# Kernel tuning notes

Measured on AMD Instinct MI355X. Metric: run time of the kernel, lower is better.

The kernel has to match this reference:

```python
import jax, jax.numpy as jnp
import numpy as np

B, S, H, DH = 8, 2048, 4, 32
D = H * DH  # all_head_size = true_hidden_size = 128


def setup_inputs() -> dict:
    key = jax.random.key(0)
    ks = jax.random.split(key, 9)
    inp = {
        "query_tensor": jax.random.normal(ks[0], (B, S, D), dtype=jnp.float32),
        "key_tensor": jax.random.normal(ks[1], (B, S, D), dtype=jnp.float32),
        "value_tensor": jax.random.normal(ks[2], (B, S, D), dtype=jnp.float32),
        "attention_mask": jnp.zeros((B, 1, 1, S), dtype=jnp.float32),
        "head_mask": jnp.ones((1, H, 1, 1), dtype=jnp.float32),
        "Wq": jax.random.normal(ks[3], (D, D), dtype=jnp.float32) * 0.02,
        "bq": jnp.zeros((D,), dtype=jnp.float32),
        "Wk": jax.random.normal(ks[4], (D, D), dtype=jnp.float32) * 0.02,
        "bk": jnp.zeros((D,), dtype=jnp.float32),
        "Wv": jax.random.normal(ks[5], (D, D), dtype=jnp.float32) * 0.02,
        "bv": jnp.zeros((D,), dtype=jnp.float32),
    }
    return inp


def _split_heads(x):
    # (B, S, D) -> (B, H, S, DH)
    return x.reshape(B, S, H, DH).transpose(0, 2, 1, 3)


def reference(query_tensor, key_tensor, value_tensor, attention_mask, head_mask,
              Wq, bq, Wk, bk, Wv, bv):
    q = _split_heads(query_tensor @ Wq + bq)   # (B,H,S,DH)
    k = _split_heads(key_tensor @ Wk + bk)
    v = _split_heads(value_tensor @ Wv + bv)

    scale = 1.0 / jnp.sqrt(jnp.float32(DH))
    scores = jnp.einsum("bhqd,bhkd->bhqk", q, k) * scale + attention_mask
    probs = jax.nn.softmax(scores, axis=-1)
    # dropout is identity at inference (training=False)
    probs = probs * head_mask
    ctx = jnp.einsum("bhqk,bhkd->bhqd", probs, v)  # (B,H,S,DH)
    ctx = ctx.transpose(0, 2, 1, 3).reshape(B, S, D)
    return ctx
```

## Files before the change

kernel.cpp:

```cpp
#include <hip/hip_runtime.h>
#include <hip/hip_bf16.h>
#include <math.h>

#define B_ 8
#define S_ 2048
#define H_ 4
#define DH_ 32
#define D_ 128
#define BS_ (B_ * S_)
#define NT_ 32
#define LOG2E 1.4426950408889634f
#define QSCALE (0.17677669529663687f * LOG2E)

typedef float f32x4 __attribute__((ext_vector_type(4)));
typedef short s16x8 __attribute__((ext_vector_type(8)));

__device__ __forceinline__ unsigned short bf(float x) {
    return __builtin_bit_cast(unsigned short, __float2bfloat16(x));
}
__device__ __forceinline__ float bf2f(unsigned short u) {
    return __builtin_bit_cast(float, (unsigned int)u << 16);
}
__device__ __forceinline__ unsigned int pk2(float a, float b) {
    return (unsigned int)bf(a) | ((unsigned int)bf(b) << 16);
}
__device__ __forceinline__ void gll16(const void* g, void* l) {
    __builtin_amdgcn_global_load_lds(
        (const __attribute__((address_space(1))) unsigned int*)(g),
        (__attribute__((address_space(3))) unsigned int*)(l), 16, 0, 0);
}

__global__ __launch_bounds__(256) void wprep(
    const float* __restrict__ Wq, const float* __restrict__ Wk, const float* __restrict__ Wv,
    const float* __restrict__ maskg,
    unsigned short* __restrict__ Wt, unsigned short* __restrict__ Em)
{
    if (blockIdx.z == 3) {
        const int id16 = blockIdx.y * 4 + blockIdx.x;
        const int base = id16 * 1024 + threadIdx.x * 4;
        float4 m4 = *(const float4*)&maskg[base];
        ushort4 o;
        o.x = bf(__builtin_amdgcn_exp2f(m4.x * LOG2E));
        o.y = bf(__builtin_amdgcn_exp2f(m4.y * LOG2E));
        o.z = bf(__builtin_amdgcn_exp2f(m4.z * LOG2E));
        o.w = bf(__builtin_amdgcn_exp2f(m4.w * LOG2E));
        *(ushort4*)&Em[base] = o;
        return;
    }
    const float* W = (blockIdx.z == 0) ? Wq : (blockIdx.z == 1) ? Wk : Wv;
    unsigned short* Oh = Wt + (size_t)blockIdx.z * D_ * D_;
    unsigned short* Ol = Oh + 3 * D_ * D_;
    __shared__ float tf[32][36];
    const int t = threadIdx.x;
    const int kt = blockIdx.x * 32, ct = blockIdx.y * 32;
    {
        int kl = t >> 3, cl = (t & 7) * 4;
        float4 w4 = *(const float4*)&W[(size_t)(kt + kl) * D_ + ct + cl];
        tf[kl][cl + 0] = w4.x; tf[kl][cl + 1] = w4.y;
        tf[kl][cl + 2] = w4.z; tf[kl][cl + 3] = w4.w;
    }
    __syncthreads();
    {
        int cl = t >> 3, kl = (t & 7) * 4;
        ushort4 oh, ol;
        float v;
        v = tf[kl + 0][cl]; oh.x = bf(v); ol.x = bf(v - bf2f(oh.x));
        v = tf[kl + 1][cl]; oh.y = bf(v); ol.y = bf(v - bf2f(oh.y));
        v = tf[kl + 2][cl]; oh.z = bf(v); ol.z = bf(v - bf2f(oh.z));
        v = tf[kl + 3][cl]; oh.w = bf(v); ol.w = bf(v - bf2f(oh.w));
        *(ushort4*)&Oh[(size_t)(ct + cl) * D_ + kt + kl] = oh;
        *(ushort4*)&Ol[(size_t)(ct + cl) * D_ + kt + kl] = ol;
    }
}

__global__ __launch_bounds__(256) void qkv_mfma(
    const float* __restrict__ Xq, const float* __restrict__ Xk, const float* __restrict__ Xv,
    const unsigned short* __restrict__ Wt, const float* __restrict__ maskg,
    const float* __restrict__ bq, const float* __restrict__ bk, const float* __restrict__ bv,
    unsigned short* __restrict__ Qo, unsigned short* __restrict__ Ko,
    unsigned short* __restrict__ Vt)
{
    const int mode = blockIdx.z, chalf = blockIdx.y;
    const float* X; const float* bias; unsigned short* O; float scl;
    if (mode == 0)      { X = Xq; bias = bq; O = Qo; scl = QSCALE; }
    else if (mode == 1) { X = Xk; bias = bk; O = Ko; scl = 1.f; }
    else                { X = Xv; bias = bv; O = Vt; scl = 1.f; }
    const unsigned short* WmH = Wt + (size_t)mode * D_ * D_;
    const unsigned short* WmL = WmH + 3 * D_ * D_;

    __shared__ __align__(16) unsigned short xa[2 * 32 * 136];
    __shared__ __align__(16) unsigned short wt[2 * 64 * 136];

    const int t = threadIdx.x;
    const long row0 = (long)blockIdx.x * 32;

    #pragma unroll
    for (int j = 0; j < 8; j++) {
        int idx = t + 256 * j;
        int part = idx >> 10, i2 = idx & 1023;
        int r = i2 >> 4, c16 = i2 & 15;
        const unsigned short* src = part ? WmL : WmH;
        uint4 v = *(const uint4*)&src[(size_t)(chalf * 64 + r) * D_ + c16 * 8];
        *(uint4*)&wt[part * 8704 + r * 136 + c16 * 8] = v;
    }
    #pragma unroll
    for (int j = 0; j < 4; j++) {
        int idx = t + 256 * j;
        int r = idx >> 5, c4 = idx & 31;
        float4 v = *(const float4*)(X + (row0 + r) * D_ + c4 * 4);
        ushort4 ph, pl;
        ph.x = bf(v.x); pl.x = bf(v.x - bf2f(ph.x));
        ph.y = bf(v.y); pl.y = bf(v.y - bf2f(ph.y));
        ph.z = bf(v.z); pl.z = bf(v.z - bf2f(ph.z));
        ph.w = bf(v.w); pl.w = bf(v.w - bf2f(ph.w));
        *(ushort4*)&xa[r * 136 + c4 * 4] = ph;
        *(ushort4*)&xa[4352 + r * 136 + c4 * 4] = pl;
    }
    __syncthreads();

    const int w = t >> 6, lane = t & 63, lo = lane & 15, hi = lane >> 4;
    const int mf = w >> 1, nb = (w & 1) * 2;
    f32x4 acc[2] = {};
    #pragma unroll
    for (int kk = 0; kk < 4; kk++) {
        const int ko = kk * 32 + hi * 8;
        s16x8 ah = *(const s16x8*)&xa[(mf * 16 + lo) * 136 + ko];
        s16x8 al = *(const s16x8*)&xa[4352 + (mf * 16 + lo) * 136 + ko];
        #pragma unroll
        for (int n2 = 0; n2 < 2; n2++) {
            const int nf = nb + n2;
            s16x8 bh2 = *(const s16x8*)&wt[(nf * 16 + lo) * 136 + ko];
            s16x8 bl2 = *(const s16x8*)&wt[8704 + (nf * 16 + lo) * 136 + ko];
            acc[n2] = __builtin_amdgcn_mfma_f32_16x16x32_bf16(ah, bh2, acc[n2], 0, 0, 0);
            acc[n2] = __builtin_amdgcn_mfma_f32_16x16x32_bf16(al, bh2, acc[n2], 0, 0, 0);
            acc[n2] = __builtin_amdgcn_mfma_f32_16x16x32_bf16(ah, bl2, acc[n2], 0, 0, 0);
        }
    }
    __syncthreads();

    if (mode < 2) {
        #pragma unroll
        for (int n2 = 0; n2 < 2; n2++) {
            int c_l = (nb + n2) * 16 + lo;
            float bb = bias[chalf * 64 + c_l];
            #pragma unroll
            for (int r = 0; r < 4; r++) {
                int s = mf * 16 + hi * 4 + r;
                xa[s * 72 + c_l] = bf((acc[n2][r] + bb) * scl);
            }
        }
        __syncthreads();
        int s = t >> 3, part = t & 7;
        int c_g = chalf * 64 + part * 8;
        int h = c_g >> 5, d = c_g & 31;
        long b_i = (row0 + s) >> 11, s_i = (row0 + s) & 2047;
        unsigned short* orow = O + ((b_i * H_ + h) * (long)S_ + s_i) * DH_ + d;
        *(uint4*)orow = *(const uint4*)&xa[s * 72 + part * 8];
    } else {
        const long b_i = row0 >> 11;
        const long s0g = row0 & 2047;
        float emr[4];
        #pragma unroll
        for (int r = 0; r < 4; r++) {
            const int s_l = mf * 16 + hi * 4 + r;
            emr[r] = __builtin_amdgcn_exp2f(maskg[b_i * S_ + s0g + s_l] * LOG2E);
        }
        #pragma unroll
        for (int n2 = 0; n2 < 2; n2++) {
            int c_l = (nb + n2) * 16 + lo;
            float bb = bias[chalf * 64 + c_l];
            #pragma unroll
            for (int r = 0; r < 4; r++) {
                int s = mf * 16 + hi * 4 + r;
                xa[c_l * 68 + s] = bf((acc[n2][r] + bb) * emr[r]);
            }
        }
        __syncthreads();
        if (t < 128) {
            int c_l = t >> 1, sh2 = (t & 1) * 16;
            int c_g = chalf * 64 + c_l;
            int h = c_g >> 5, d = c_g & 31;
            long s_i = s0g + sh2;
            unsigned short* orow = O + ((b_i * H_ + h) * (long)DH_ + d) * S_ + s_i;
            uint2 p0 = *(const uint2*)&xa[c_l * 68 + sh2 + 0];
            uint2 p1 = *(const uint2*)&xa[c_l * 68 + sh2 + 4];
            uint2 p2 = *(const uint2*)&xa[c_l * 68 + sh2 + 8];
            uint2 p3 = *(const uint2*)&xa[c_l * 68 + sh2 + 12];
            *(uint4*)&orow[0] = make_uint4(p0.x, p0.y, p1.x, p1.y);
            *(uint4*)&orow[8] = make_uint4(p2.x, p2.y, p3.x, p3.y);
        }
    }
}

__global__ __launch_bounds__(256) void flash_mfma(
    const unsigned short* __restrict__ Qg, const unsigned short* __restrict__ Kg,
    const unsigned short* __restrict__ Vtg, const unsigned short* __restrict__ Emg,
    const float* __restrict__ head_mask, float* __restrict__ Out)
{
    __shared__ __align__(16) unsigned short ks[2][64][32];
    __shared__ __align__(16) unsigned short vs[2][32][72];
    __shared__ __align__(16) unsigned short ps[4][16][72];

    const int t = threadIdx.x, w = t >> 6, lane = t & 63;
    const int lo = lane & 15, hi = lane >> 4;

    const int lid = blockIdx.x;
    const int xcd = lid & 7, ser = lid >> 3;
    const int bh = xcd + 8 * (ser >> 5);
    const int qi = ser & 31;
    const int b = bh >> 2, h = bh & 3;

    const size_t kvbase = (size_t)bh * S_ * DH_;
    const size_t vtbase = (size_t)bh * DH_ * S_;
    const unsigned short* emb = Emg + (size_t)b * S_;
    const int q0 = qi * 64 + w * 16;

    s16x8 qf = *(const s16x8*)(Qg + kvbase + (size_t)(q0 + lo) * DH_ + hi * 8);

    const float hm = head_mask[h];
    const int vd = t >> 3, vk = (t & 7) * 8;
    const int krow = lane >> 2, kchunk = (lane & 3) ^ (krow & 3);
    const size_t koff = (size_t)(w * 16 + krow) * DH_ + kchunk * 8;

    gll16(Kg + kvbase + koff, &ks[0][w * 16][0]);
    *(uint4*)&vs[0][vd][vk] = *(const uint4*)(Vtg + vtbase + (size_t)vd * S_ + vk);
    __syncthreads();

    f32x4 ctx[2] = {};
    f32x4 lacc = {};
    const f32x4 z4 = {0.f, 0.f, 0.f, 0.f};
    uint4 vreg;

    const int kread = (hi ^ (lo & 3)) * 8;

    for (int tile = 0; tile < NT_; tile++) {
        const int cur = tile & 1, nxt = cur ^ 1;

        if (tile < NT_ - 1) {
            gll16(Kg + kvbase + (size_t)(tile + 1) * 64 * DH_ + koff, &ks[nxt][w * 16][0]);
            vreg = *(const uint4*)(Vtg + vtbase + (size_t)vd * S_ + (tile + 1) * 64 + vk);
        }
        s16x8 ef0 = *(const s16x8*)(emb + tile * 64 + hi * 8);
        s16x8 ef1 = *(const s16x8*)(emb + tile * 64 + 32 + hi * 8);

        __builtin_amdgcn_s_setprio(1);
        #pragma unroll
        for (int mt = 0; mt < 4; mt++) {
            s16x8 kf = *(const s16x8*)&ks[cur][mt * 16 + lo][kread];
            f32x4 d = __builtin_amdgcn_mfma_f32_16x16x32_bf16(kf, qf, z4, 0, 0, 0);
            float p0 = __builtin_amdgcn_exp2f(d[0]);
            float p1 = __builtin_amdgcn_exp2f(d[1]);
            float p2 = __builtin_amdgcn_exp2f(d[2]);
            float p3 = __builtin_amdgcn_exp2f(d[3]);
            uint2 u = make_uint2(pk2(p0, p1), pk2(p2, p3));
            *(uint2*)&ps[w][lo][mt * 16 + hi * 4] = u;
        }
        __builtin_amdgcn_s_setprio(0);

        __builtin_amdgcn_s_setprio(1);
        #pragma unroll
        for (int k2 = 0; k2 < 2; k2++) {
            s16x8 pa = *(const s16x8*)&ps[w][lo][k2 * 32 + hi * 8];
            lacc = __builtin_amdgcn_mfma_f32_16x16x32_bf16(pa, k2 ? ef1 : ef0, lacc, 0, 0, 0);
            #pragma unroll
            for (int nd = 0; nd < 2; nd++) {
                s16x8 vb = *(const s16x8*)&vs[cur][nd * 16 + lo][k2 * 32 + hi * 8];
                ctx[nd] = __builtin_amdgcn_mfma_f32_16x16x32_bf16(pa, vb, ctx[nd], 0, 0, 0);
            }
        }
        __builtin_amdgcn_s_setprio(0);

        if (tile < NT_ - 1) {
            *(uint4*)&vs[nxt][vd][vk] = vreg;
            __syncthreads();
        }
    }

    f32x4 inv;
    #pragma unroll
    for (int r = 0; r < 4; r++) inv[r] = hm / lacc[r];
    #pragma unroll
    for (int nd = 0; nd < 2; nd++) {
        #pragma unroll
        for (int r = 0; r < 4; r++) {
            size_t sq = (size_t)q0 + hi * 4 + r;
            Out[((size_t)b * S_ + sq) * D_ + h * DH_ + nd * 16 + lo] = ctx[nd][r] * inv[r];
        }
    }
}

extern "C" void kernel_launch(void* const* d_in, const int* in_sizes, int n_in,
                              void* d_out, int out_size, void* d_ws, size_t ws_size,
                              hipStream_t stream) {
    const float* Xq   = (const float*)d_in[0];
    const float* Xk   = (const float*)d_in[1];
    const float* Xv   = (const float*)d_in[2];
    const float* mask = (const float*)d_in[3];
    const float* hm   = (const float*)d_in[4];
    const float* Wq   = (const float*)d_in[5];
    const float* bq   = (const float*)d_in[6];
    const float* Wk   = (const float*)d_in[7];
    const float* bk   = (const float*)d_in[8];
    const float* Wv   = (const float*)d_in[9];
    const float* bv   = (const float*)d_in[10];
    float* out = (float*)d_out;

    unsigned short* Qo = (unsigned short*)d_ws;
    unsigned short* Ko = Qo + (size_t)2097152;
    unsigned short* Vt = Ko + (size_t)2097152;
    unsigned short* Wt = Vt + (size_t)2097152;
    unsigned short* Em = Wt + (size_t)98304;

    wprep<<<dim3(4, 4, 4), 256, 0, stream>>>(Wq, Wk, Wv, mask, Wt, Em);
    qkv_mfma<<<dim3(BS_ / 32, 2, 3), 256, 0, stream>>>(Xq, Xk, Xv, Wt, mask, bq, bk, bv, Qo, Ko, Vt);
    flash_mfma<<<dim3(1024), 256, 0, stream>>>(Qo, Ko, Vt, Em, hm, out);
}
```

Baseline: 62.84 us.

## Rewrite flash attention with 32x32 MFMA, register K, permlane P reuse, additive mask

Switches the attention kernel from 16x16x32 to 32x32x16 bf16 MFMA tiles, with each wave handling 32 query rows and each block 128 queries, which halves the grid. K fragments are now loaded straight into registers instead of through LDS, and probabilities are reshuffled in registers with v_permlane32_swap rather than staged through an LDS buffer. The mask becomes an additive log2 term inside exp2 instead of a multiplicative factor applied to V and the row sum, and the row sum is computed by an MFMA against a ones vector. This removes LDS round-trips and barriers for P and K, at the cost of higher register pressure, a grid of 512 blocks, and duplicated MFMA work for the denominator.

```diff
diff --git a/kernel.cpp b/kernel.cpp
--- a/kernel.cpp
+++ b/kernel.cpp
@@ -12,8 +12,9 @@
 #define LOG2E 1.4426950408889634f
 #define QSCALE (0.17677669529663687f * LOG2E)
 
-typedef float f32x4 __attribute__((ext_vector_type(4)));
-typedef short s16x8 __attribute__((ext_vector_type(8)));
+typedef float f32x4  __attribute__((ext_vector_type(4)));
+typedef float f32x16 __attribute__((ext_vector_type(16)));
+typedef short s16x8  __attribute__((ext_vector_type(8)));
 
 __device__ __forceinline__ unsigned short bf(float x) {
     return __builtin_bit_cast(unsigned short, __float2bfloat16(x));
@@ -24,27 +25,21 @@
 __device__ __forceinline__ unsigned int pk2(float a, float b) {
     return (unsigned int)bf(a) | ((unsigned int)bf(b) << 16);
 }
-__device__ __forceinline__ void gll16(const void* g, void* l) {
-    __builtin_amdgcn_global_load_lds(
-        (const __attribute__((address_space(1))) unsigned int*)(g),
-        (__attribute__((address_space(3))) unsigned int*)(l), 16, 0, 0);
+__device__ __forceinline__ void pswap(unsigned int& a, unsigned int& b) {
+    asm volatile("v_permlane32_swap_b32 %0, %1" : "+v"(a), "+v"(b));
 }
 
 __global__ __launch_bounds__(256) void wprep(
     const float* __restrict__ Wq, const float* __restrict__ Wk, const float* __restrict__ Wv,
     const float* __restrict__ maskg,
-    unsigned short* __restrict__ Wt, unsigned short* __restrict__ Em)
+    unsigned short* __restrict__ Wt, float* __restrict__ Eml)
 {
     if (blockIdx.z == 3) {
         const int id16 = blockIdx.y * 4 + blockIdx.x;
         const int base = id16 * 1024 + threadIdx.x * 4;
         float4 m4 = *(const float4*)&maskg[base];
-        ushort4 o;
-        o.x = bf(__builtin_amdgcn_exp2f(m4.x * LOG2E));
-        o.y = bf(__builtin_amdgcn_exp2f(m4.y * LOG2E));
-        o.z = bf(__builtin_amdgcn_exp2f(m4.z * LOG2E));
-        o.w = bf(__builtin_amdgcn_exp2f(m4.w * LOG2E));
-        *(ushort4*)&Em[base] = o;
+        float4 o = make_float4(m4.x * LOG2E, m4.y * LOG2E, m4.z * LOG2E, m4.w * LOG2E);
+        *(float4*)&Eml[base] = o;
         return;
     }
     const float* W = (blockIdx.z == 0) ? Wq : (blockIdx.z == 1) ? Wk : Wv;
@@ -75,7 +70,7 @@
 
 __global__ __launch_bounds__(256) void qkv_mfma(
     const float* __restrict__ Xq, const float* __restrict__ Xk, const float* __restrict__ Xv,
-    const unsigned short* __restrict__ Wt, const float* __restrict__ maskg,
+    const unsigned short* __restrict__ Wt,
     const float* __restrict__ bq, const float* __restrict__ bk, const float* __restrict__ bv,
     unsigned short* __restrict__ Qo, unsigned short* __restrict__ Ko,
     unsigned short* __restrict__ Vt)
@@ -159,12 +154,6 @@
     } else {
         const long b_i = row0 >> 11;
         const long s0g = row0 & 2047;
-        float emr[4];
-        #pragma unroll
-        for (int r = 0; r < 4; r++) {
-            const int s_l = mf * 16 + hi * 4 + r;
-            emr[r] = __builtin_amdgcn_exp2f(maskg[b_i * S_ + s0g + s_l] * LOG2E);
-        }
         #pragma unroll
         for (int n2 = 0; n2 < 2; n2++) {
             int c_l = (nb + n2) * 16 + lo;
@@ -172,7 +161,7 @@
             #pragma unroll
             for (int r = 0; r < 4; r++) {
                 int s = mf * 16 + hi * 4 + r;
-                xa[c_l * 68 + s] = bf((acc[n2][r] + bb) * emr[r]);
+                xa[c_l * 68 + s] = bf(acc[n2][r] + bb);
             }
         }
         __syncthreads();
@@ -194,98 +183,112 @@
 
 __global__ __launch_bounds__(256) void flash_mfma(
     const unsigned short* __restrict__ Qg, const unsigned short* __restrict__ Kg,
-    const unsigned short* __restrict__ Vtg, const unsigned short* __restrict__ Emg,
+    const unsigned short* __restrict__ Vtg, const float* __restrict__ Eml,
     const float* __restrict__ head_mask, float* __restrict__ Out)
 {
-    __shared__ __align__(16) unsigned short ks[2][64][32];
     __shared__ __align__(16) unsigned short vs[2][32][72];
-    __shared__ __align__(16) unsigned short ps[4][16][72];
 
     const int t = threadIdx.x, w = t >> 6, lane = t & 63;
-    const int lo = lane & 15, hi = lane >> 4;
+    const int l31 = lane & 31, hw = lane >> 5;
 
     const int lid = blockIdx.x;
     const int xcd = lid & 7, ser = lid >> 3;
-    const int bh = xcd + 8 * (ser >> 5);
-    const int qi = ser & 31;
+    const int bh = xcd + 8 * (ser >> 4);
+    const int qi = ser & 15;
     const int b = bh >> 2, h = bh & 3;
 
     const size_t kvbase = (size_t)bh * S_ * DH_;
     const size_t vtbase = (size_t)bh * DH_ * S_;
-    const unsigned short* emb = Emg + (size_t)b * S_;
-    const int q0 = qi * 64 + w * 16;
-
-    s16x8 qf = *(const s16x8*)(Qg + kvbase + (size_t)(q0 + lo) * DH_ + hi * 8);
-
+    const float* emlb = Eml + (size_t)b * S_;
+    const int q0 = qi * 128 + w * 32;
     const float hm = head_mask[h];
+
+    const unsigned short* qp = Qg + kvbase + (size_t)(q0 + l31) * DH_ + hw * 8;
+    const s16x8 qf0 = *(const s16x8*)qp;
+    const s16x8 qf1 = *(const s16x8*)(qp + 16);
+
+    const unsigned short* kfp = Kg + kvbase + (size_t)l31 * DH_ + hw * 8;
+    s16x8 kf00 = *(const s16x8*)(kfp);
+    s16x8 kf01 = *(const s16x8*)(kfp + 16);
+    s16x8 kf10 = *(const s16x8*)(kfp + 1024);
+    s16x8 kf11 = *(const s16x8*)(kfp + 1040);
+
     const int vd = t >> 3, vk = (t & 7) * 8;
-    const int krow = lane >> 2, kchunk = (lane & 3) ^ (krow & 3);
-    const size_t koff = (size_t)(w * 16 + krow) * DH_ + kchunk * 8;
-
-    gll16(Kg + kvbase + koff, &ks[0][w * 16][0]);
     *(uint4*)&vs[0][vd][vk] = *(const uint4*)(Vtg + vtbase + (size_t)vd * S_ + vk);
     __syncthreads();
 
-    f32x4 ctx[2] = {};
-    f32x4 lacc = {};
-    const f32x4 z4 = {0.f, 0.f, 0.f, 0.f};
-    uint4 vreg;
-
-    const int kread = (hi ^ (lo & 3)) * 8;
+    f32x16 ctx = {};
+    f32x16 lacc = {};
+    const f32x16 z16 = {};
+    const s16x8 ones = {0x3F80, 0x3F80, 0x3F80, 0x3F80, 0x3F80, 0x3F80, 0x3F80, 0x3F80};
 
     for (int tile = 0; tile < NT_; tile++) {
         const int cur = tile & 1, nxt = cur ^ 1;
 
+        s16x8 kn00, kn01, kn10, kn11; uint4 vreg;
         if (tile < NT_ - 1) {
-            gll16(Kg + kvbase + (size_t)(tile + 1) * 64 * DH_ + koff, &ks[nxt][w * 16][0]);
+            const unsigned short* kp2 = kfp + (size_t)(tile + 1) * 2048;
+            kn00 = *(const s16x8*)(kp2);
+            kn01 = *(const s16x8*)(kp2 + 16);
+            kn10 = *(const s16x8*)(kp2 + 1024);
+            kn11 = *(const s16x8*)(kp2 + 1040);
             vreg = *(const uint4*)(Vtg + vtbase + (size_t)vd * S_ + (tile + 1) * 64 + vk);
         }
-        s16x8 ef0 = *(const s16x8*)(emb + tile * 64 + hi * 8);
-        s16x8 ef1 = *(const s16x8*)(emb + tile * 64 + 32 + hi * 8);
-
-        __builtin_amdgcn_s_setprio(1);
-        #pragma unroll
-        for (int mt = 0; mt < 4; mt++) {
-            s16x8 kf = *(const s16x8*)&ks[cur][mt * 16 + lo][kread];
-            f32x4 d = __builtin_amdgcn_mfma_f32_16x16x32_bf16(kf, qf, z4, 0, 0, 0);
-            float p0 = __builtin_amdgcn_exp2f(d[0]);
-            float p1 = __builtin_amdgcn_exp2f(d[1]);
-            float p2 = __builtin_amdgcn_exp2f(d[2]);
-            float p3 = __builtin_amdgcn_exp2f(d[3]);
-            uint2 u = make_uint2(pk2(p0, p1), pk2(p2, p3));
-            *(uint2*)&ps[w][lo][mt * 16 + hi * 4] = u;
-        }
-        __builtin_amdgcn_s_setprio(0);
-
-        __builtin_amdgcn_s_setprio(1);
-        #pragma unroll
-        for (int k2 = 0; k2 < 2; k2++) {
-            s16x8 pa = *(const s16x8*)&ps[w][lo][k2 * 32 + hi * 8];
-            lacc = __builtin_amdgcn_mfma_f32_16x16x32_bf16(pa, k2 ? ef1 : ef0, lacc, 0, 0, 0);
+        const float* emt = emlb + tile * 64 + hw * 4;
+        f32x4 ea[4], eb[4];
+        #pragma unroll
+        for (int g = 0; g < 4; g++) {
+            ea[g] = *(const f32x4*)(emt + g * 8);
+            eb[g] = *(const f32x4*)(emt + 32 + g * 8);
+        }
+
+        #pragma unroll
+        for (int kgrp = 0; kgrp < 2; kgrp++) {
+            const s16x8 ka = kgrp ? kf10 : kf00;
+            const s16x8 kb = kgrp ? kf11 : kf01;
+
+            __builtin_amdgcn_s_setprio(1);
+            f32x16 s = __builtin_amdgcn_mfma_f32_32x32x16_bf16(ka, qf0, z16, 0, 0, 0);
+            s = __builtin_amdgcn_mfma_f32_32x32x16_bf16(kb, qf1, s, 0, 0, 0);
+            __builtin_amdgcn_s_setprio(0);
+
+            unsigned int pd[8];
             #pragma unroll
-            for (int nd = 0; nd < 2; nd++) {
-                s16x8 vb = *(const s16x8*)&vs[cur][nd * 16 + lo][k2 * 32 + hi * 8];
-                ctx[nd] = __builtin_amdgcn_mfma_f32_16x16x32_bf16(pa, vb, ctx[nd], 0, 0, 0);
+            for (int j = 0; j < 8; j++) {
+                const int r0 = 2 * j, r1 = 2 * j + 1;
+                const float e0 = kgrp ? eb[r0 >> 2][r0 & 3] : ea[r0 >> 2][r0 & 3];
+                const float e1 = kgrp ? eb[r1 >> 2][r1 & 3] : ea[r1 >> 2][r1 & 3];
+                const float p0 = __builtin_amdgcn_exp2f(s[r0] + e0);
+                const float p1 = __builtin_amdgcn_exp2f(s[r1] + e1);
+                pd[j] = pk2(p0, p1);
             }
-        }
-        __builtin_amdgcn_s_setprio(0);
+            pswap(pd[0], pd[2]); pswap(pd[1], pd[3]);
+            pswap(pd[4], pd[6]); pswap(pd[5], pd[7]);
+            const s16x8 pa0 = __builtin_bit_cast(s16x8, make_uint4(pd[0], pd[1], pd[2], pd[3]));
+            const s16x8 pa1 = __builtin_bit_cast(s16x8, make_uint4(pd[4], pd[5], pd[6], pd[7]));
+
+            __builtin_amdgcn_s_setprio(1);
+            const s16x8 vb0 = *(const s16x8*)&vs[cur][l31][kgrp * 32 + hw * 8];
+            ctx  = __builtin_amdgcn_mfma_f32_32x32x16_bf16(pa0, vb0, ctx, 0, 0, 0);
+            lacc = __builtin_amdgcn_mfma_f32_32x32x16_bf16(pa0, ones, lacc, 0, 0, 0);
+            const s16x8 vb1 = *(const s16x8*)&vs[cur][l31][kgrp * 32 + 16 + hw * 8];
+            ctx  = __builtin_amdgcn_mfma_f32_32x32x16_bf16(pa1, vb1, ctx, 0, 0, 0);
+            lacc = __builtin_amdgcn_mfma_f32_32x32x16_bf16(pa1, ones, lacc, 0, 0, 0);
+            __builtin_amdgcn_s_setprio(0);
+        }
 
         if (tile < NT_ - 1) {
             *(uint4*)&vs[nxt][vd][vk] = vreg;
             __syncthreads();
-        }
-    }
-
-    f32x4 inv;
+            kf00 = kn00; kf01 = kn01; kf10 = kn10; kf11 = kn11;
+        }
+    }
+
     #pragma unroll
-    for (int r = 0; r < 4; r++) inv[r] = hm / lacc[r];
-    #pragma unroll
-    for (int nd = 0; nd < 2; nd++) {
-        #pragma unroll
-        for (int r = 0; r < 4; r++) {
-            size_t sq = (size_t)q0 + hi * 4 + r;
-            Out[((size_t)b * S_ + sq) * D_ + h * DH_ + nd * 16 + lo] = ctx[nd][r] * inv[r];
-        }
+    for (int r = 0; r < 16; r++) {
+        const int qrow = (r & 3) + 8 * (r >> 2) + 4 * hw;
+        const float inv = hm / lacc[r];
+        Out[((size_t)b * S_ + q0 + qrow) * D_ + h * DH_ + l31] = ctx[r] * inv;
     }
 }
 
@@ -309,9 +312,9 @@
     unsigned short* Ko = Qo + (size_t)2097152;
     unsigned short* Vt = Ko + (size_t)2097152;
     unsigned short* Wt = Vt + (size_t)2097152;
-    unsigned short* Em = Wt + (size_t)98304;
-
-    wprep<<<dim3(4, 4, 4), 256, 0, stream>>>(Wq, Wk, Wv, mask, Wt, Em);
-    qkv_mfma<<<dim3(BS_ / 32, 2, 3), 256, 0, stream>>>(Xq, Xk, Xv, Wt, mask, bq, bk, bv, Qo, Ko, Vt);
-    flash_mfma<<<dim3(1024), 256, 0, stream>>>(Qo, Ko, Vt, Em, hm, out);
-}
+    float*          Eml = (float*)((char*)d_ws + 12779520);
+
+    wprep<<<dim3(4, 4, 4), 256, 0, stream>>>(Wq, Wk, Wv, mask, Wt, Eml);
+    qkv_mfma<<<dim3(BS_ / 32, 2, 3), 256, 0, stream>>>(Xq, Xk, Xv, Wt, bq, bk, bv, Qo, Ko, Vt);
+    flash_mfma<<<dim3(512), 256, 0, stream>>>(Qo, Ko, Vt, Eml, hm, out);
+}
```

New measurement: 73.61 us. +17.1%, slower.

## Rewrite attention with 32x32 MFMA, fragment-ordered K/V layout and split-K waves

Applied to the files above, without the earlier changes.

The QKV projection now writes K and V straight into MFMA fragment order, so the attention kernel loads its operands from global memory into registers with no LDS staging or barriers in the main loop. The attention kernel switches to 32x32x16 MFMA with 32 query rows per block. The four waves split the key range and are combined through an LDS reduction at the end. P is repacked with v_cvt_pk_bf16_f32 and v_permlane32_swap instead of a round trip through LDS. This removes the per-tile LDS traffic and syncs, at the cost of a doubled grid, a final cross-wave reduction, and more register pressure.

```diff
diff --git a/kernel.cpp b/kernel.cpp
--- a/kernel.cpp
+++ b/kernel.cpp
@@ -8,12 +8,12 @@
 #define DH_ 32
 #define D_ 128
 #define BS_ (B_ * S_)
-#define NT_ 32
 #define LOG2E 1.4426950408889634f
 #define QSCALE (0.17677669529663687f * LOG2E)
 
-typedef float f32x4 __attribute__((ext_vector_type(4)));
-typedef short s16x8 __attribute__((ext_vector_type(8)));
+typedef float f32x4  __attribute__((ext_vector_type(4)));
+typedef float f32x16 __attribute__((ext_vector_type(16)));
+typedef short s16x8  __attribute__((ext_vector_type(8)));
 
 __device__ __forceinline__ unsigned short bf(float x) {
     return __builtin_bit_cast(unsigned short, __float2bfloat16(x));
@@ -22,13 +22,19 @@
     return __builtin_bit_cast(float, (unsigned int)u << 16);
 }
 __device__ __forceinline__ unsigned int pk2(float a, float b) {
-    return (unsigned int)bf(a) | ((unsigned int)bf(b) << 16);
-}
-__device__ __forceinline__ void gll16(const void* g, void* l) {
-    __builtin_amdgcn_global_load_lds(
-        (const __attribute__((address_space(1))) unsigned int*)(g),
-        (__attribute__((address_space(3))) unsigned int*)(l), 16, 0, 0);
-}
+    unsigned int r;
+    asm("v_cvt_pk_bf16_f32 %0, %1, %2" : "=v"(r) : "v"(a), "v"(b));
+    return r;
+}
+__device__ __forceinline__ void pswap(unsigned int& a, unsigned int& b) {
+    asm volatile("v_permlane32_swap_b32 %0, %1" : "+v"(a), "+v"(b));
+}
+
+#define OFF_Q  0u
+#define OFF_K  2097152u
+#define OFF_V  4194304u
+#define OFF_W  6291456u
+#define OFF_E  6389760u
 
 __global__ __launch_bounds__(256) void wprep(
     const float* __restrict__ Wq, const float* __restrict__ Wk, const float* __restrict__ Wv,
@@ -77,14 +83,14 @@
     const float* __restrict__ Xq, const float* __restrict__ Xk, const float* __restrict__ Xv,
     const unsigned short* __restrict__ Wt, const float* __restrict__ maskg,
     const float* __restrict__ bq, const float* __restrict__ bk, const float* __restrict__ bv,
-    unsigned short* __restrict__ Qo, unsigned short* __restrict__ Ko,
-    unsigned short* __restrict__ Vt)
+    unsigned short* __restrict__ Qo, unsigned short* __restrict__ Kf,
+    unsigned short* __restrict__ Vf)
 {
     const int mode = blockIdx.z, chalf = blockIdx.y;
-    const float* X; const float* bias; unsigned short* O; float scl;
-    if (mode == 0)      { X = Xq; bias = bq; O = Qo; scl = QSCALE; }
-    else if (mode == 1) { X = Xk; bias = bk; O = Ko; scl = 1.f; }
-    else                { X = Xv; bias = bv; O = Vt; scl = 1.f; }
+    const float* X; const float* bias; float scl;
+    if (mode == 0)      { X = Xq; bias = bq; scl = QSCALE; }
+    else if (mode == 1) { X = Xk; bias = bk; scl = 1.f; }
+    else                { X = Xv; bias = bv; scl = 1.f; }
     const unsigned short* WmH = Wt + (size_t)mode * D_ * D_;
     const unsigned short* WmL = WmH + 3 * D_ * D_;
 
@@ -138,6 +144,9 @@
     }
     __syncthreads();
 
+    const long b_i = row0 >> 11;
+    const long s0g = row0 & 2047;
+
     if (mode < 2) {
         #pragma unroll
         for (int n2 = 0; n2 < 2; n2++) {
@@ -152,13 +161,19 @@
         __syncthreads();
         int s = t >> 3, part = t & 7;
         int c_g = chalf * 64 + part * 8;
-        int h = c_g >> 5, d = c_g & 31;
-        long b_i = (row0 + s) >> 11, s_i = (row0 + s) & 2047;
-        unsigned short* orow = O + ((b_i * H_ + h) * (long)S_ + s_i) * DH_ + d;
-        *(uint4*)orow = *(const uint4*)&xa[s * 72 + part * 8];
+        int h = c_g >> 5, dd = c_g & 31;
+        long s_i = s0g + s;
+        int bh = (int)(b_i * H_ + h);
+        uint4 val = *(const uint4*)&xa[s * 72 + part * 8];
+        if (mode == 0) {
+            *(uint4*)(Qo + ((size_t)bh * S_ + s_i) * DH_ + dd) = val;
+        } else {
+            int fr = dd >> 4, hwd = (dd >> 3) & 1;
+            size_t off = ((((size_t)bh * 64 + (s_i >> 5)) * 2 + fr) * 64
+                          + (s_i & 31) + hwd * 32) * 8;
+            *(uint4*)(Kf + off) = val;
+        }
     } else {
-        const long b_i = row0 >> 11;
-        const long s0g = row0 & 2047;
         float emr[4];
         #pragma unroll
         for (int r = 0; r < 4; r++) {
@@ -179,112 +194,116 @@
         if (t < 128) {
             int c_l = t >> 1, sh2 = (t & 1) * 16;
             int c_g = chalf * 64 + c_l;
-            int h = c_g >> 5, d = c_g & 31;
-            long s_i = s0g + sh2;
-            unsigned short* orow = O + ((b_i * H_ + h) * (long)DH_ + d) * S_ + s_i;
+            int h = c_g >> 5, dd = c_g & 31;
+            long key0 = s0g + sh2;
+            int bh = (int)(b_i * H_ + h);
+            size_t base = (((size_t)bh * 128 + (key0 >> 4)) * 64 + dd) * 8;
             uint2 p0 = *(const uint2*)&xa[c_l * 68 + sh2 + 0];
             uint2 p1 = *(const uint2*)&xa[c_l * 68 + sh2 + 4];
             uint2 p2 = *(const uint2*)&xa[c_l * 68 + sh2 + 8];
             uint2 p3 = *(const uint2*)&xa[c_l * 68 + sh2 + 12];
-            *(uint4*)&orow[0] = make_uint4(p0.x, p0.y, p1.x, p1.y);
-            *(uint4*)&orow[8] = make_uint4(p2.x, p2.y, p3.x, p3.y);
-        }
-    }
-}
-
-__global__ __launch_bounds__(256) void flash_mfma(
-    const unsigned short* __restrict__ Qg, const unsigned short* __restrict__ Kg,
-    const unsigned short* __restrict__ Vtg, const unsigned short* __restrict__ Emg,
+            *(uint4*)(Vf + base)       = make_uint4(p0.x, p0.y, p1.x, p1.y);
+            *(uint4*)(Vf + base + 256) = make_uint4(p2.x, p2.y, p3.x, p3.y);
+        }
+    }
+}
+
+__global__ __launch_bounds__(256, 4) void flash_mfma(
+    const unsigned short* __restrict__ Qg, const unsigned short* __restrict__ Kfg,
+    const unsigned short* __restrict__ Vfg, const unsigned short* __restrict__ Emg,
     const float* __restrict__ head_mask, float* __restrict__ Out)
 {
-    __shared__ __align__(16) unsigned short ks[2][64][32];
-    __shared__ __align__(16) unsigned short vs[2][32][72];
-    __shared__ __align__(16) unsigned short ps[4][16][72];
+    __shared__ float ms[2][64][33];
 
     const int t = threadIdx.x, w = t >> 6, lane = t & 63;
-    const int lo = lane & 15, hi = lane >> 4;
+    const int l31 = lane & 31, hw = lane >> 5;
 
     const int lid = blockIdx.x;
     const int xcd = lid & 7, ser = lid >> 3;
-    const int bh = xcd + 8 * (ser >> 5);
-    const int qi = ser & 31;
+    const int bh = xcd * 4 + (ser >> 6);
+    const int qi = ser & 63;
     const int b = bh >> 2, h = bh & 3;
-
-    const size_t kvbase = (size_t)bh * S_ * DH_;
-    const size_t vtbase = (size_t)bh * DH_ * S_;
-    const unsigned short* emb = Emg + (size_t)b * S_;
-    const int q0 = qi * 64 + w * 16;
-
-    s16x8 qf = *(const s16x8*)(Qg + kvbase + (size_t)(q0 + lo) * DH_ + hi * 8);
-
-    const float hm = head_mask[h];
-    const int vd = t >> 3, vk = (t & 7) * 8;
-    const int krow = lane >> 2, kchunk = (lane & 3) ^ (krow & 3);
-    const size_t koff = (size_t)(w * 16 + krow) * DH_ + kchunk * 8;
-
-    gll16(Kg + kvbase + koff, &ks[0][w * 16][0]);
-    *(uint4*)&vs[0][vd][vk] = *(const uint4*)(Vtg + vtbase + (size_t)vd * S_ + vk);
-    __syncthreads();
-
-    f32x4 ctx[2] = {};
-    f32x4 lacc = {};
-    const f32x4 z4 = {0.f, 0.f, 0.f, 0.f};
-    uint4 vreg;
-
-    const int kread = (hi ^ (lo & 3)) * 8;
-
-    for (int tile = 0; tile < NT_; tile++) {
-        const int cur = tile & 1, nxt = cur ^ 1;
-
-        if (tile < NT_ - 1) {
-            gll16(Kg + kvbase + (size_t)(tile + 1) * 64 * DH_ + koff, &ks[nxt][w * 16][0]);
-            vreg = *(const uint4*)(Vtg + vtbase + (size_t)vd * S_ + (tile + 1) * 64 + vk);
-        }
-        s16x8 ef0 = *(const s16x8*)(emb + tile * 64 + hi * 8);
-        s16x8 ef1 = *(const s16x8*)(emb + tile * 64 + 32 + hi * 8);
-
-        __builtin_amdgcn_s_setprio(1);
-        #pragma unroll
-        for (int mt = 0; mt < 4; mt++) {
-            s16x8 kf = *(const s16x8*)&ks[cur][mt * 16 + lo][kread];
-            f32x4 d = __builtin_amdgcn_mfma_f32_16x16x32_bf16(kf, qf, z4, 0, 0, 0);
-            float p0 = __builtin_amdgcn_exp2f(d[0]);
-            float p1 = __builtin_amdgcn_exp2f(d[1]);
-            float p2 = __builtin_amdgcn_exp2f(d[2]);
-            float p3 = __builtin_amdgcn_exp2f(d[3]);
-            uint2 u = make_uint2(pk2(p0, p1), pk2(p2, p3));
-            *(uint2*)&ps[w][lo][mt * 16 + hi * 4] = u;
-        }
-        __builtin_amdgcn_s_setprio(0);
-
-        __builtin_amdgcn_s_setprio(1);
-        #pragma unroll
-        for (int k2 = 0; k2 < 2; k2++) {
-            s16x8 pa = *(const s16x8*)&ps[w][lo][k2 * 32 + hi * 8];
-            lacc = __builtin_amdgcn_mfma_f32_16x16x32_bf16(pa, k2 ? ef1 : ef0, lacc, 0, 0, 0);
-            #pragma unroll
-            for (int nd = 0; nd < 2; nd++) {
-                s16x8 vb = *(const s16x8*)&vs[cur][nd * 16 + lo][k2 * 32 + hi * 8];
-                ctx[nd] = __builtin_amdgcn_mfma_f32_16x16x32_bf16(pa, vb, ctx[nd], 0, 0, 0);
-            }
-        }
-        __builtin_amdgcn_s_setprio(0);
-
-        if (tile < NT_ - 1) {
-            *(uint4*)&vs[nxt][vd][vk] = vreg;
-            __syncthreads();
-        }
-    }
-
-    f32x4 inv;
-    #pragma unroll
-    for (int r = 0; r < 4; r++) inv[r] = hm / lacc[r];
-    #pragma unroll
-    for (int nd = 0; nd < 2; nd++) {
-        #pragma unroll
-        for (int r = 0; r < 4; r++) {
-            size_t sq = (size_t)q0 + hi * 4 + r;
-            Out[((size_t)b * S_ + sq) * D_ + h * DH_ + nd * 16 + lo] = ctx[nd][r] * inv[r];
+    const int q0 = qi * 32;
+
+    const unsigned short* qp = Qg + ((size_t)bh * S_ + q0 + l31) * DH_ + hw * 8;
+    const s16x8 qf0 = *(const s16x8*)qp;
+    const s16x8 qf1 = *(const s16x8*)(qp + 16);
+
+    const unsigned short* kp = Kfg + (size_t)bh * 65536 + (size_t)w * 1024 + (size_t)lane * 8;
+    const unsigned short* vp = Vfg + (size_t)bh * 65536 + (size_t)w * 1024 + (size_t)lane * 8;
+    const unsigned short* ep = Emg + (size_t)b * S_ + w * 32 + hw * 8;
+
+    s16x8 kf0 = *(const s16x8*)kp;
+    s16x8 kf1 = *(const s16x8*)(kp + 512);
+    s16x8 vf0 = *(const s16x8*)vp;
+    s16x8 vf1 = *(const s16x8*)(vp + 512);
+
+    f32x16 ctx = {}, lacc = {};
+    const f32x16 z16 = {};
+
+    for (int tile = 0; tile < 16; tile++) {
+        s16x8 kn0, kn1, vn0, vn1;
+        if (tile < 15) {
+            const unsigned short* kp2 = kp + (size_t)(tile + 1) * 4096;
+            const unsigned short* vp2 = vp + (size_t)(tile + 1) * 4096;
+            kn0 = *(const s16x8*)kp2;
+            kn1 = *(const s16x8*)(kp2 + 512);
+            vn0 = *(const s16x8*)vp2;
+            vn1 = *(const s16x8*)(vp2 + 512);
+        }
+        const s16x8 ef0 = *(const s16x8*)(ep + tile * 128);
+        const s16x8 ef1 = *(const s16x8*)(ep + tile * 128 + 16);
+
+        f32x16 s = __builtin_amdgcn_mfma_f32_32x32x16_bf16(kf0, qf0, z16, 0, 0, 0);
+        s = __builtin_amdgcn_mfma_f32_32x32x16_bf16(kf1, qf1, s, 0, 0, 0);
+
+        unsigned int pd[8];
+        #pragma unroll
+        for (int j = 0; j < 8; j++) {
+            const float p0 = __builtin_amdgcn_exp2f(s[2 * j]);
+            const float p1 = __builtin_amdgcn_exp2f(s[2 * j + 1]);
+            pd[j] = pk2(p0, p1);
+        }
+        pswap(pd[0], pd[2]); pswap(pd[1], pd[3]);
+        pswap(pd[4], pd[6]); pswap(pd[5], pd[7]);
+        const s16x8 pa0 = __builtin_bit_cast(s16x8, make_uint4(pd[0], pd[1], pd[2], pd[3]));
+        const s16x8 pa1 = __builtin_bit_cast(s16x8, make_uint4(pd[4], pd[5], pd[6], pd[7]));
+
+        ctx  = __builtin_amdgcn_mfma_f32_32x32x16_bf16(pa0, vf0, ctx, 0, 0, 0);
+        lacc = __builtin_amdgcn_mfma_f32_32x32x16_bf16(pa0, ef0, lacc, 0, 0, 0);
+        ctx  = __builtin_amdgcn_mfma_f32_32x32x16_bf16(pa1, vf1, ctx, 0, 0, 0);
+        lacc = __builtin_amdgcn_mfma_f32_32x32x16_bf16(pa1, ef1, lacc, 0, 0, 0);
+
+        if (tile < 15) { kf0 = kn0; kf1 = kn1; vf0 = vn0; vf1 = vn1; }
+    }
+
+    if (w >= 2) {
+        float* d = &ms[w - 2][lane][0];
+        #pragma unroll
+        for (int r = 0; r < 16; r++) { d[r] = ctx[r]; d[16 + r] = lacc[r]; }
+    }
+    __syncthreads();
+    if (w < 2) {
+        const float* sr = &ms[w][lane][0];
+        #pragma unroll
+        for (int r = 0; r < 16; r++) { ctx[r] += sr[r]; lacc[r] += sr[16 + r]; }
+    }
+    __syncthreads();
+    if (w == 1) {
+        float* d = &ms[0][lane][0];
+        #pragma unroll
+        for (int r = 0; r < 16; r++) { d[r] = ctx[r]; d[16 + r] = lacc[r]; }
+    }
+    __syncthreads();
+    if (w == 0) {
+        const float* sr = &ms[0][lane][0];
+        #pragma unroll
+        for (int r = 0; r < 16; r++) { ctx[r] += sr[r]; lacc[r] += sr[16 + r]; }
+        const float hm = head_mask[h];
+        #pragma unroll
+        for (int r = 0; r < 16; r++) {
+            const int qrow = (r & 3) + 8 * (r >> 2) + 4 * hw;
+            Out[((size_t)b * S_ + q0 + qrow) * D_ + h * DH_ + l31] = ctx[r] * hm / lacc[r];
         }
     }
 }
@@ -305,13 +324,15 @@
     const float* bv   = (const float*)d_in[10];
     float* out = (float*)d_out;
 
-    unsigned short* Qo = (unsigned short*)d_ws;
-    unsigned short* Ko = Qo + (size_t)2097152;
-    unsigned short* Vt = Ko + (size_t)2097152;
-    unsigned short* Wt = Vt + (size_t)2097152;
-    unsigned short* Em = Wt + (size_t)98304;
+    unsigned short* ws = (unsigned short*)d_ws;
+    unsigned short* Qo = ws + OFF_Q;
+    unsigned short* Kf = ws + OFF_K;
+    unsigned short* Vf = ws + OFF_V;
+    unsigned short* Wt = ws + OFF_W;
+    unsigned short* Em = ws + OFF_E;
 
     wprep<<<dim3(4, 4, 4), 256, 0, stream>>>(Wq, Wk, Wv, mask, Wt, Em);
-    qkv_mfma<<<dim3(BS_ / 32, 2, 3), 256, 0, stream>>>(Xq, Xk, Xv, Wt, mask, bq, bk, bv, Qo, Ko, Vt);
-    flash_mfma<<<dim3(1024), 256, 0, stream>>>(Qo, Ko, Vt, Em, hm, out);
-}
+    qkv_mfma<<<dim3(BS_ / 32, 2, 3), 256, 0, stream>>>(Xq, Xk, Xv, Wt, mask,
+                                                       bq, bk, bv, Qo, Kf, Vf);
+    flash_mfma<<<dim3(2048), 256, 0, stream>>>(Qo, Kf, Vf, Em, hm, out);
+}
```

Measured after the change: 54.61 us. 1.15x faster.
